# Kernel optimization log

Measured on AMD Instinct MI355X. Metric: run time of the kernel, lower is better.

Reference implementation:

```python
import jax, jax.numpy as jnp
import numpy as np

NU = 256      # numunits
NH = 32       # torch.split chunk size == head dim in this code
B = 128
S = 256


def _linear_tanh(x, W, b):
    # torch nn.Linear: y = x @ W.T + b, followed by tanh
    return jnp.tanh(x @ W.T + b)


def _split_heads(x):
    # torch.split(x, NH, dim=-1) then cat(dim=0): chunk c occupies rows [c*B, (c+1)*B)
    b, s, d = x.shape
    c = d // NH
    return x.reshape(b, s, c, NH).transpose(2, 0, 1, 3).reshape(c * b, s, NH)


def _merge_heads(x, b):
    # torch.split(x, batchsize, dim=0) then cat(dim=-1): inverse of _split_heads
    cb, s, hd = x.shape
    c = cb // b
    return x.reshape(c, b, s, hd).transpose(1, 2, 0, 3).reshape(b, s, c * hd)


def _attention(Q, K, V):
    d_k = jnp.asarray(K.shape[2], Q.dtype) ** 0.5
    scores = jnp.einsum('nqd,nkd->nqk', Q, K) / d_k
    # NB: original uses F.softmax(scores) with no dim on a 3D tensor ->
    # torch legacy default is dim=0. We reproduce that exactly.
    p_attn = jax.nn.softmax(scores, axis=0)
    return jnp.einsum('nqk,nkd->nqd', p_attn, V)


def setup_inputs() -> dict:
    key = jax.random.key(0)
    ks = jax.random.split(key, 24)
    def w(k):
        return jax.random.normal(k, (NU, NU), dtype=jnp.float32) * 0.02
    def bvec(k):
        return jax.random.normal(k, (NU,), dtype=jnp.float32) * 0.02
    inp = {
        'queries1': jax.random.normal(ks[0], (B, S, NU), dtype=jnp.float32),
        'queries2': jax.random.normal(ks[1], (B, S, NU), dtype=jnp.float32),
        'queries3': jax.random.normal(ks[2], (B, S, NU), dtype=jnp.float32),
        'adj': jax.random.randint(ks[3], (B,), 0, B, dtype=jnp.int64),
        'WQ': w(ks[4]),  'bQ': bvec(ks[5]),
        'WV': w(ks[6]),  'bV': bvec(ks[7]),
        'WQ3': w(ks[8]), 'bQ3': bvec(ks[9]),
        'WK3': w(ks[10]), 'bK3': bvec(ks[11]),
        'WV3': w(ks[12]), 'bV3': bvec(ks[13]),
        'WQ4': w(ks[14]), 'bQ4': bvec(ks[15]),
        'WV4': w(ks[16]), 'bV4': bvec(ks[17]),
        'W5': jax.random.normal(ks[18], (NU, 4 * NU), dtype=jnp.float32) * 0.02,
        'b5': bvec(ks[19]),
    }
    return inp


def reference(queries1, queries2, queries3, adj,
              WQ, bQ, WV, bV, WQ3, bQ3, WK3, bK3, WV3, bV3,
              WQ4, bQ4, WV4, bV4, W5, b5):
    b = queries1.shape[0]
    # per-row batch gather: queries4[i] = queries3[adj[i]]
    queries4 = queries3[adj]

    Q1 = _split_heads(_linear_tanh(queries1, WQ, bQ))
    Q2 = _split_heads(_linear_tanh(queries2, WQ, bQ))
    Q3 = _split_heads(_linear_tanh(queries3, WQ3, bQ3))
    Q4 = _split_heads(_linear_tanh(queries4, WQ4, bQ4))
    K3 = _split_heads(_linear_tanh(queries3, WK3, bK3))
    V1 = _split_heads(_linear_tanh(queries1, WV, bV))
    V2 = _split_heads(_linear_tanh(queries2, WV, bV))
    V3 = _split_heads(_linear_tanh(queries3, WV3, bV3))
    V4 = _split_heads(_linear_tanh(queries4, WV4, bV4))

    o1 = _merge_heads(_attention(Q1, K3, V1), b)
    o2 = _merge_heads(_attention(Q2, K3, V2), b)
    o3 = _merge_heads(_attention(Q3, K3, V3), b)
    o4 = _merge_heads(_attention(Q4, K3, V4), b)

    o5 = jnp.tanh(jnp.concatenate([o1, o2, o3, o4], axis=-1) @ W5.T + b5)
    return (o1, o2, o5, o3)
```

## Files before the change

kernel.cpp:

```cpp
#include <hip/hip_runtime.h>


typedef __attribute__((ext_vector_type(4))) float f32x4;
typedef __attribute__((ext_vector_type(8))) short bf16x8;

#define LOG2E 1.4426950408889634f
#define SM_SCALE (1.4426950408889634f / 5.656854249492381f)

#define CVT_PK(d, lo, hi) \
    asm("v_cvt_pk_bf16_f32 %0, %1, %2" : "=v"(d) : "v"(lo), "v"(hi))
#define SWAP32(x, y) \
    asm("v_permlane32_swap_b32 %0, %1" : "+v"(x), "+v"(y))
#define SWAP16(x, y) \
    asm("v_permlane16_swap_b32 %0, %1" : "+v"(x), "+v"(y))
#define GLOAD16(g, p) __builtin_amdgcn_global_load_lds( \
    (const __attribute__((address_space(1))) void*)(g), \
    (__attribute__((address_space(3))) void*)(p), 16, 0, 0)

__device__ __forceinline__ unsigned short f2bf(float x) {
    union { float f; unsigned u; } v; v.f = x;
    unsigned r = v.u + 0x7FFFu + ((v.u >> 16) & 1u);
    return (unsigned short)(r >> 16);
}

__device__ __forceinline__ float bf2f(unsigned short x) {
    union { unsigned u; float f; } v; v.u = ((unsigned)x) << 16;
    return v.f;
}

__device__ __forceinline__ float fast_tanh(float x) {
    float e = __builtin_amdgcn_exp2f(x * (2.0f * LOG2E));
    return 1.0f - 2.0f * __builtin_amdgcn_rcpf(e + 1.0f);
}

__device__ __forceinline__ f32x4 mfma_bf16(bf16x8 a, bf16x8 b, f32x4 c) {
    return __builtin_amdgcn_mfma_f32_16x16x32_bf16(a, b, c, 0, 0, 0);
}

__global__ __launch_bounds__(256) void k_convert_w(
    const float* w0, const float* w1, const float* w2, const float* w3,
    const float* w4, const float* w5, const float* w6, const float* w7,
    unsigned short* out)
{
    int i = blockIdx.x * 256 + threadIdx.x;
    if (i >= 720896) return;
    float v;
    if (i < 458752) {
        int r = i >> 16, j = i & 65535;
        const float* s =
            (r == 0) ? w0 : (r == 1) ? w1 : (r == 2) ? w2 :
            (r == 3) ? w3 : (r == 4) ? w4 : (r == 5) ? w5 : w6;
        v = s[j];
    } else {
        v = w7[i - 458752];
    }
    out[i] = (short)f2bf(v);
}

__global__ __launch_bounds__(256) void k_convert_x(
    const float* __restrict__ q1, const float* __restrict__ q2,
    const float* __restrict__ q3, unsigned short* __restrict__ Xb)
{
    const int gi = (blockIdx.x * 256 + threadIdx.x) * 8;
    const float* s = (gi < 8388608) ? q1 : (gi < 16777216) ? q2 : q3;
    const int off = gi & 8388607;
    float4 f0 = *(const float4*)(s + off);
    float4 f1 = *(const float4*)(s + off + 4);
    unsigned a0, a1, a2, a3;
    CVT_PK(a0, f0.x, f0.y);
    CVT_PK(a1, f0.z, f0.w);
    CVT_PK(a2, f1.x, f1.y);
    CVT_PK(a3, f1.z, f1.w);
    uint4 pk; pk.x = a0; pk.y = a1; pk.z = a2; pk.w = a3;
    *(uint4*)(Xb + gi) = pk;
}

__global__ __launch_bounds__(512, 4) void k_linear(
    const unsigned short* __restrict__ Xb, const int* __restrict__ adj,
    const unsigned short* __restrict__ wb,
    const float* __restrict__ bQ, const float* __restrict__ bV,
    const float* __restrict__ bQ3, const float* __restrict__ bK3,
    const float* __restrict__ bV3, const float* __restrict__ bQ4,
    const float* __restrict__ bV4,
    unsigned short* __restrict__ lin)
{
    __shared__ __align__(16) short lds[24576];
    const int bid0 = blockIdx.x;
    const int swz = (bid0 & 7) * 320 + (bid0 >> 3);
    const int var = swz >> 9;
    const int rem = swz & 511;
    const int m0 = (rem >> 1) * 128, n0 = (rem & 1) * 128;

    const unsigned short* X = Xb + (size_t)((var == 0) ? 0 : (var == 1) ? 1 : 2) * 8388608;
    const bool gather = (var == 4);
    const int nout = (var == 3) ? 1 : 2;

    int widx0, widx1 = 0, zidx0, zidx1 = 0;
    const float* bp0;
    const float* bp1 = bQ;
    if (var == 0)      { widx0=0; widx1=1; zidx0=0; zidx1=5; bp0=bQ;  bp1=bV;  }
    else if (var == 1) { widx0=0; widx1=1; zidx0=1; zidx1=6; bp0=bQ;  bp1=bV;  }
    else if (var == 2) { widx0=2; widx1=3; zidx0=2; zidx1=4; bp0=bQ3; bp1=bK3; }
    else if (var == 3) { widx0=4;          zidx0=7;          bp0=bV3;          }
    else               { widx0=5; widx1=6; zidx0=3; zidx1=8; bp0=bQ4; bp1=bV4; }

    const int tid = threadIdx.x;
    const int w = tid >> 6, l = tid & 63;
    const int wm = w >> 2, wn = w & 3;
    const int lr = l & 15, lk = (l >> 4) * 8, lq = (l >> 4) * 4;

    const int rowT = (w << 4) + (l >> 2);
    const int colT = (l & 3) << 3;
    const int gm = m0 + rowT;
    const int sm = gather ? (adj[gm >> 8] * 256 + (gm & 255)) : gm;
    const unsigned short* aG  = X + (size_t)sm * 256 + colT;
    const unsigned short* b0G = wb + (size_t)widx0 * 65536 + (size_t)(n0 + rowT) * 256 + colT;
    const unsigned short* b1G = wb + (size_t)widx1 * 65536 + (size_t)(n0 + rowT) * 256 + colT;
    char* ldsB = (char*)lds;
    const int wslice = w << 10;

    f32x4 acc[2][4][2] = {};

    GLOAD16(aG, ldsB + wslice);
    GLOAD16(b0G, ldsB + 8192 + wslice);
    if (nout == 2) GLOAD16(b1G, ldsB + 16384 + wslice);
    __syncthreads();

    for (int st = 0; st < 8; ++st) {
        const int p = st & 1;
        if (st < 7) {
            const int ko = (st + 1) * 32;
            char* nb = ldsB + (p ^ 1) * 24576;
            GLOAD16(aG + ko, nb + wslice);
            GLOAD16(b0G + ko, nb + 8192 + wslice);
            if (nout == 2) GLOAD16(b1G + ko, nb + 16384 + wslice);
        }
        const short* base = lds + p * 12288;
        bf16x8 af[4], bf0v[2], bf1v[2];
        #pragma unroll
        for (int i = 0; i < 4; ++i)
            af[i] = *(const bf16x8*)&base[(wm * 64 + i * 16 + lr) * 32 + lk];
        #pragma unroll
        for (int j = 0; j < 2; ++j)
            bf0v[j] = *(const bf16x8*)&base[4096 + (wn * 32 + j * 16 + lr) * 32 + lk];
        if (nout == 2)
            #pragma unroll
            for (int j = 0; j < 2; ++j)
                bf1v[j] = *(const bf16x8*)&base[8192 + (wn * 32 + j * 16 + lr) * 32 + lk];
        #pragma unroll
        for (int i = 0; i < 4; ++i)
            #pragma unroll
            for (int j = 0; j < 2; ++j)
                acc[0][i][j] = mfma_bf16(af[i], bf0v[j], acc[0][i][j]);
        if (nout == 2)
            #pragma unroll
            for (int i = 0; i < 4; ++i)
                #pragma unroll
                for (int j = 0; j < 2; ++j)
                    acc[1][i][j] = mfma_bf16(af[i], bf1v[j], acc[1][i][j]);
        __syncthreads();
    }

    #pragma unroll
    for (int t = 0; t < 2; ++t)
        if (t < nout) {
            const float* bp = t ? bp1 : bp0;
            const int zi = t ? zidx1 : zidx0;
            const float qs = (zi <= 3) ? SM_SCALE : 1.0f;
            float bv[2];
            #pragma unroll
            for (int j = 0; j < 2; ++j)
                bv[j] = bp[n0 + wn * 32 + j * 16 + lr];
            #pragma unroll
            for (int i = 0; i < 4; ++i)
                #pragma unroll
                for (int j = 0; j < 2; ++j)
                    #pragma unroll
                    for (int r = 0; r < 4; ++r)
                        lds[(wm * 64 + i * 16 + lq + r) * 136 + wn * 32 + j * 16 + lr] =
                            (short)f2bf(fast_tanh(acc[t][i][j][r] + bv[j]) * qs);
            __syncthreads();
            unsigned short* Y = lin + (size_t)zi * 8388608;
            #pragma unroll
            for (int it2 = 0; it2 < 4; ++it2) {
                const int c = tid + it2 * 512;
                const int row = c >> 4, col8 = (c & 15) * 8;
                *(bf16x8*)(Y + (size_t)(m0 + row) * 256 + n0 + col8) =
                    *(const bf16x8*)&lds[row * 136 + col8];
            }
            __syncthreads();
        }
}

__global__ __launch_bounds__(256) void k_denom(
    const unsigned short* __restrict__ Qa, const unsigned short* __restrict__ Qb2,
    const unsigned short* __restrict__ Qc, const unsigned short* __restrict__ Qd,
    const unsigned short* __restrict__ Kb, unsigned short* __restrict__ partial2)
{
    __shared__ __align__(16) short Qs[2][128 * 40];
    __shared__ __align__(16) short Ks[2][128 * 40];
    const int tid = threadIdx.x, w = tid >> 6, l = tid & 63;
    const int q0 = (blockIdx.x >> 1) * 128, k0 = (blockIdx.x & 1) * 128;
    const int g = blockIdx.y, a = blockIdx.z;
    const unsigned short* Qb = (a == 0) ? Qa : (a == 1) ? Qb2 : (a == 2) ? Qc : Qd;
    const int lr = l & 15, lk = (l >> 4) * 8;

    f32x4 eacc[2][8] = {};
    for (int it = 0; it < 32; it += 2) {
        __syncthreads();
        #pragma unroll
        for (int u = 0; u < 2; ++u) {
            const int n = g * 32 + it + u;
            const int c = n >> 7, b = n & 127;
            const size_t base = (size_t)b * 65536 + (size_t)c * 32;
            for (int ci = tid; ci < 512; ci += 256) {
                int r = ci >> 2, ch = ci & 3;
                *(bf16x8*)&Qs[u][r * 40 + ch * 8] =
                    *(const bf16x8*)(Qb + base + (size_t)(q0 + r) * 256 + ch * 8);
                *(bf16x8*)&Ks[u][r * 40 + ch * 8] =
                    *(const bf16x8*)(Kb + base + (size_t)(k0 + r) * 256 + ch * 8);
            }
        }
        __syncthreads();
        #pragma unroll
        for (int u = 0; u < 2; ++u) {
            bf16x8 aq[2], bk[8];
            #pragma unroll
            for (int i = 0; i < 2; ++i)
                aq[i] = *(const bf16x8*)&Qs[u][(w * 32 + i * 16 + lr) * 40 + lk];
            #pragma unroll
            for (int j = 0; j < 8; ++j)
                bk[j] = *(const bf16x8*)&Ks[u][(j * 16 + lr) * 40 + lk];
            #pragma unroll
            for (int i = 0; i < 2; ++i)
                #pragma unroll
                for (int j = 0; j < 8; ++j) {
                    f32x4 s = mfma_bf16(aq[i], bk[j], (f32x4){0.f, 0.f, 0.f, 0.f});
                    #pragma unroll
                    for (int r = 0; r < 4; ++r)
                        eacc[i][j][r] += __builtin_amdgcn_exp2f(s[r]);
                }
        }
    }
    const size_t pbase = (((size_t)a * 32 + g) << 16) + (size_t)blockIdx.x * 16384;
    #pragma unroll
    for (int cch = 0; cch < 8; ++cch) {
        const int ii = cch >> 2, jp = (cch & 3) * 2;
        union { unsigned short s[8]; bf16x8 v; } U;
        #pragma unroll
        for (int m = 0; m < 8; ++m)
            U.s[m] = f2bf(eacc[ii][jp + (m >> 2)][m & 3]);
        *(bf16x8*)&partial2[pbase + cch * 2048 + tid * 8] = U.v;
    }
}

__global__ __launch_bounds__(256) void k_reduce(
    const unsigned short* __restrict__ partial2, float* __restrict__ dinvP)
{
    const int a = blockIdx.y;
    const int gi = blockIdx.x * 256 + threadIdx.x;
    const unsigned short* p = partial2 + (size_t)a * 2097152 + gi;
    float s = 0.f;
    #pragma unroll
    for (int g = 0; g < 32; ++g) s += bf2f(p[(size_t)g * 65536]);
    const int tile = gi >> 14, rem2 = gi & 16383;
    const int cch = rem2 >> 11, tid2 = (rem2 >> 3) & 255, m = rem2 & 7;
    const int ii = cch >> 2, j = (cch & 3) * 2 + (m >> 2), r = m & 3;
    const int w2 = tid2 >> 6, l2 = tid2 & 63;
    const int q = (tile >> 1) * 128 + w2 * 32 + ii * 16 + ((l2 >> 4) * 4) + r;
    const int k = (tile & 1) * 128 + j * 16 + (l2 & 15);
    const int w_ = q >> 6, iq = (q >> 4) & 3, q16 = q & 15;
    const int kp = k >> 5, jj = (k >> 4) & 1, h = (k >> 2) & 3, rr = k & 3;
    const int off = (((((((w_ * 8 + kp) * 4 + iq) * 2 + jj) * 4 + h) * 16) + q16) * 4) + rr;
    dinvP[((size_t)a << 16) + off] = 1.0f / s;
}

__global__ __launch_bounds__(256) void k_attn(
    const unsigned short* __restrict__ Q1, const unsigned short* __restrict__ Q2,
    const unsigned short* __restrict__ Q3, const unsigned short* __restrict__ Q4,
    const unsigned short* __restrict__ Kb,
    const unsigned short* __restrict__ V1, const unsigned short* __restrict__ V2,
    const unsigned short* __restrict__ V3, const unsigned short* __restrict__ V4,
    const float* __restrict__ dinvP,
    float* __restrict__ outBase, unsigned short* __restrict__ ob4)
{
    __shared__ __align__(16) short Vt[32 * 264];
    __shared__ __align__(16) short Ks[256 * 40];
    const int tid = threadIdx.x, w = tid >> 6, l = tid & 63;
    const int bid = blockIdx.x;
    const int swz = (bid & 7) * 512 + (bid >> 3);
    const int a = swz & 3, n = swz >> 2;
    const int c = n >> 7, b = n & 127;
    const int q16 = l & 15, h = l >> 4;
    const size_t base = (size_t)b * 65536 + (size_t)c * 32;

    const unsigned short* Qb = (a == 0) ? Q1 : (a == 1) ? Q2 : (a == 2) ? Q3 : Q4;
    const unsigned short* Vb = (a == 0) ? V1 : (a == 1) ? V2 : (a == 2) ? V3 : V4;
    const f32x4* dw = (const f32x4*)(dinvP + ((size_t)a << 16)) + l + (size_t)w * 4096;
    float* outp = outBase + (size_t)((a == 2) ? 3 : a) * 8388608;

    {
        const unsigned short* vp = Vb + base + (size_t)tid * 256;
        const unsigned short* kp_ = Kb + base + (size_t)tid * 256;
        bf16x8 v0 = *(const bf16x8*)(vp);
        bf16x8 v1 = *(const bf16x8*)(vp + 8);
        bf16x8 v2 = *(const bf16x8*)(vp + 16);
        bf16x8 v3 = *(const bf16x8*)(vp + 24);
        bf16x8 k0 = *(const bf16x8*)(kp_);
        bf16x8 k1 = *(const bf16x8*)(kp_ + 8);
        bf16x8 k2 = *(const bf16x8*)(kp_ + 16);
        bf16x8 k3 = *(const bf16x8*)(kp_ + 24);
        *(bf16x8*)&Ks[tid * 40 + 0]  = k0;
        *(bf16x8*)&Ks[tid * 40 + 8]  = k1;
        *(bf16x8*)&Ks[tid * 40 + 16] = k2;
        *(bf16x8*)&Ks[tid * 40 + 24] = k3;
        #pragma unroll
        for (int e = 0; e < 8; ++e) {
            Vt[(0  + e) * 264 + tid] = v0[e];
            Vt[(8  + e) * 264 + tid] = v1[e];
            Vt[(16 + e) * 264 + tid] = v2[e];
            Vt[(24 + e) * 264 + tid] = v3[e];
        }
    }
    __syncthreads();

    const int q0 = w * 64;
    bf16x8 bq[4];
    #pragma unroll
    for (int i = 0; i < 4; ++i)
        bq[i] = *(const bf16x8*)(Qb + base + (size_t)(q0 + i * 16 + q16) * 256 + h * 8);

    f32x4 dc0 = dw[0];
    f32x4 dc1 = dw[64];

    f32x4 oacc[4][2] = {};
    for (int kp = 0; kp < 8; ++kp) {
        const int kk0 = kp * 32;
        bf16x8 akA = *(const bf16x8*)&Ks[(kk0 + q16) * 40 + h * 8];
        bf16x8 akB = *(const bf16x8*)&Ks[(kk0 + 16 + q16) * 40 + h * 8];
        bf16x8 vb0 = *(const bf16x8*)&Vt[(0  + q16) * 264 + kk0 + h * 8];
        bf16x8 vb1 = *(const bf16x8*)&Vt[(16 + q16) * 264 + kk0 + h * 8];
        #pragma unroll
        for (int i = 0; i < 4; ++i) {
            const int t = kp * 4 + i;
            f32x4 dn0 = dc0, dn1 = dc1;
            if (t < 31) {
                dn0 = dw[(size_t)(t + 1) * 128];
                dn1 = dw[(size_t)(t + 1) * 128 + 64];
            }
            __builtin_amdgcn_s_setprio(1);
            f32x4 s0 = mfma_bf16(akA, bq[i], (f32x4){0.f, 0.f, 0.f, 0.f});
            f32x4 s1 = mfma_bf16(akB, bq[i], (f32x4){0.f, 0.f, 0.f, 0.f});
            __builtin_amdgcn_s_setprio(0);
            float p0 = __builtin_amdgcn_exp2f(s0[0]) * dc0[0];
            float p1 = __builtin_amdgcn_exp2f(s0[1]) * dc0[1];
            float p2 = __builtin_amdgcn_exp2f(s0[2]) * dc0[2];
            float p3 = __builtin_amdgcn_exp2f(s0[3]) * dc0[3];
            float p4 = __builtin_amdgcn_exp2f(s1[0]) * dc1[0];
            float p5 = __builtin_amdgcn_exp2f(s1[1]) * dc1[1];
            float p6 = __builtin_amdgcn_exp2f(s1[2]) * dc1[2];
            float p7 = __builtin_amdgcn_exp2f(s1[3]) * dc1[3];
            unsigned r0, r1, r2, r3;
            CVT_PK(r0, p0, p1);
            CVT_PK(r1, p2, p3);
            CVT_PK(r2, p4, p5);
            CVT_PK(r3, p6, p7);
            SWAP32(r0, r2); SWAP16(r0, r2);
            SWAP32(r1, r3); SWAP16(r1, r3);
            union { unsigned u[4]; bf16x8 v; } F;
            F.u[0] = r0; F.u[1] = r1; F.u[2] = r2; F.u[3] = r3;
            __builtin_amdgcn_s_setprio(1);
            oacc[i][0] = mfma_bf16(F.v, vb0, oacc[i][0]);
            oacc[i][1] = mfma_bf16(F.v, vb1, oacc[i][1]);
            __builtin_amdgcn_s_setprio(0);
            dc0 = dn0; dc1 = dn1;
        }
    }
    if (a == 3) {
        #pragma unroll
        for (int i = 0; i < 4; ++i)
            #pragma unroll
            for (int d = 0; d < 2; ++d)
                #pragma unroll
                for (int r = 0; r < 4; ++r) {
                    int q = q0 + i * 16 + h * 4 + r;
                    int dc = d * 16 + q16;
                    ob4[(size_t)b * 65536 + (size_t)q * 256 + c * 32 + dc] =
                        f2bf(oacc[i][d][r]);
                }
    } else {
        #pragma unroll
        for (int i = 0; i < 4; ++i)
            #pragma unroll
            for (int d = 0; d < 2; ++d)
                #pragma unroll
                for (int r = 0; r < 4; ++r) {
                    int q = q0 + i * 16 + h * 4 + r;
                    int dc = d * 16 + q16;
                    outp[(size_t)b * 65536 + (size_t)q * 256 + c * 32 + dc] =
                        oacc[i][d][r];
                }
    }
}

__global__ __launch_bounds__(512, 2) void k_final(
    const float* __restrict__ p0, const float* __restrict__ p1,
    const float* __restrict__ p2, const unsigned short* __restrict__ p3,
    const unsigned short* __restrict__ W5b, const float* __restrict__ b5,
    float* __restrict__ out)
{
    __shared__ __align__(16) short As[128 * 72];
    __shared__ __align__(16) short Bs[256 * 72];
    const int tid = threadIdx.x, w = tid >> 6, l = tid & 63;
    const int wm = w >> 2, wn = w & 3;
    const int m0 = blockIdx.x * 128;
    const int lr = l & 15, lk = (l >> 4) * 8, lq = (l >> 4) * 4;

    f32x4 acc[4][4] = {};
    for (int step = 0; step < 16; ++step) {
        const int k0 = step * 64;
        const int kc = k0 & 255;
        __syncthreads();
        if (step < 12) {
            const float* P = (step < 4) ? p0 : (step < 8) ? p1 : p2;
            #pragma unroll
            for (int it = 0; it < 2; ++it) {
                const int cc = tid + it * 512;
                const int row = cc >> 3, ch = cc & 7;
                const float* src = P + (size_t)(m0 + row) * 256 + kc + ch * 8;
                float4 f0 = *(const float4*)src;
                float4 f1 = *(const float4*)(src + 4);
                unsigned a0, a1, a2, a3;
                CVT_PK(a0, f0.x, f0.y);
                CVT_PK(a1, f0.z, f0.w);
                CVT_PK(a2, f1.x, f1.y);
                CVT_PK(a3, f1.z, f1.w);
                uint4 pk; pk.x = a0; pk.y = a1; pk.z = a2; pk.w = a3;
                *(uint4*)&As[row * 72 + ch * 8] = pk;
            }
        } else {
            #pragma unroll
            for (int it = 0; it < 2; ++it) {
                const int cc = tid + it * 512;
                const int row = cc >> 3, ch = cc & 7;
                *(bf16x8*)&As[row * 72 + ch * 8] =
                    *(const bf16x8*)(p3 + (size_t)(m0 + row) * 256 + kc + ch * 8);
            }
        }
        #pragma unroll
        for (int it = 0; it < 4; ++it) {
            const int cc = tid + it * 512;
            const int row = cc >> 3, ch = cc & 7;
            *(bf16x8*)&Bs[row * 72 + ch * 8] =
                *(const bf16x8*)(W5b + (size_t)row * 1024 + k0 + ch * 8);
        }
        __syncthreads();
        #pragma unroll
        for (int kk = 0; kk < 2; ++kk) {
            bf16x8 af[4], bfr[4];
            #pragma unroll
            for (int i = 0; i < 4; ++i)
                af[i] = *(const bf16x8*)&As[(wm * 64 + i * 16 + lr) * 72 + kk * 32 + lk];
            #pragma unroll
            for (int j = 0; j < 4; ++j)
                bfr[j] = *(const bf16x8*)&Bs[(wn * 64 + j * 16 + lr) * 72 + kk * 32 + lk];
            #pragma unroll
            for (int i = 0; i < 4; ++i)
                #pragma unroll
                for (int j = 0; j < 4; ++j)
                    acc[i][j] = mfma_bf16(af[i], bfr[j], acc[i][j]);
        }
    }
    #pragma unroll
    for (int j = 0; j < 4; ++j) {
        int col = wn * 64 + j * 16 + lr;
        float bv = b5[col];
        #pragma unroll
        for (int i = 0; i < 4; ++i) {
            int rowb = m0 + wm * 64 + i * 16 + lq;
            #pragma unroll
            for (int r = 0; r < 4; ++r)
                out[(size_t)(rowb + r) * 256 + col] =
                    fast_tanh(acc[i][j][r] + bv);
        }
    }
}

extern "C" void kernel_launch(void* const* d_in, const int* in_sizes, int n_in,
                              void* d_out, int out_size, void* d_ws, size_t ws_size,
                              hipStream_t stream)
{
    const float* q1  = (const float*)d_in[0];
    const float* q2  = (const float*)d_in[1];
    const float* q3  = (const float*)d_in[2];
    const int*   adj = (const int*)d_in[3];
    const float* WQ  = (const float*)d_in[4];  const float* bQ  = (const float*)d_in[5];
    const float* WV  = (const float*)d_in[6];  const float* bV  = (const float*)d_in[7];
    const float* WQ3 = (const float*)d_in[8];  const float* bQ3 = (const float*)d_in[9];
    const float* WK3 = (const float*)d_in[10]; const float* bK3 = (const float*)d_in[11];
    const float* WV3 = (const float*)d_in[12]; const float* bV3 = (const float*)d_in[13];
    const float* WQ4 = (const float*)d_in[14]; const float* bQ4 = (const float*)d_in[15];
    const float* WV4 = (const float*)d_in[16]; const float* bV4 = (const float*)d_in[17];
    const float* W5  = (const float*)d_in[18]; const float* b5  = (const float*)d_in[19];

    char* ws = (char*)d_ws;
    unsigned short* wb  = (unsigned short*)ws;
    unsigned short* W5b = wb + 458752;
    unsigned short* lin = (unsigned short*)(ws + 1441792);
    unsigned short* Q1 = lin + 0ull * 8388608;
    unsigned short* Q2 = lin + 1ull * 8388608;
    unsigned short* Q3 = lin + 2ull * 8388608;
    unsigned short* Q4 = lin + 3ull * 8388608;
    unsigned short* K3 = lin + 4ull * 8388608;
    unsigned short* V1 = lin + 5ull * 8388608;
    unsigned short* V2 = lin + 6ull * 8388608;
    unsigned short* V3 = lin + 7ull * 8388608;
    unsigned short* V4 = lin + 8ull * 8388608;
    unsigned short* partial2 = (unsigned short*)(ws + 152436736);
    float* dinvP   = (float*)(ws + 185991168);
    unsigned short* ob4 = (unsigned short*)(ws + 152436736);

    float* outf = (float*)d_out;
    float* o5p = outf + 2ull * 8388608;
    unsigned short* Xb = (unsigned short*)d_out;

    dim3 blk(256);

    hipLaunchKernelGGL(k_convert_w, dim3(2816), blk, 0, stream,
                       WQ, WV, WQ3, WK3, WV3, WQ4, WV4, W5, wb);
    hipLaunchKernelGGL(k_convert_x, dim3(12288), blk, 0, stream,
                       q1, q2, q3, Xb);

    hipLaunchKernelGGL(k_linear, dim3(2560), dim3(512), 0, stream,
                       Xb, adj, wb,
                       bQ, bV, bQ3, bK3, bV3, bQ4, bV4, lin);

    hipLaunchKernelGGL(k_denom, dim3(4, 32, 4), blk, 0, stream,
                       Q1, Q2, Q3, Q4, K3, partial2);
    hipLaunchKernelGGL(k_reduce, dim3(256, 4), blk, 0, stream, partial2, dinvP);

    hipLaunchKernelGGL(k_attn, dim3(4096), blk, 0, stream,
                       Q1, Q2, Q3, Q4, K3, V1, V2, V3, V4, dinvP,
                       outf, ob4);

    hipLaunchKernelGGL(k_final, dim3(256), dim3(512), 0, stream,
                       outf, outf + 8388608ull, outf + 3ull * 8388608, ob4,
                       W5b, b5, o5p);
}
```

Before: 288.1 us.

## Double-buffer k_denom Q/K tiles with async global-to-LDS loads

Replaces the synchronous register-staged Q/K tile loads in the softmax-denominator kernel with global_load_lds direct-to-LDS copies into a double buffer. The next head slice is prefetched while MFMA and exp2 work runs on the current one, and each iteration now needs a single barrier instead of two per pair of slices. The padded stride-40 LDS layout is dropped for an unpadded stride-32 layout, which may add LDS bank conflicts on the fragment reads. The loop also stops processing two slices per iteration.

```diff
diff --git a/kernel.cpp b/kernel.cpp
--- a/kernel.cpp
+++ b/kernel.cpp
@@ -197,51 +197,58 @@
     const unsigned short* __restrict__ Qc, const unsigned short* __restrict__ Qd,
     const unsigned short* __restrict__ Kb, unsigned short* __restrict__ partial2)
 {
-    __shared__ __align__(16) short Qs[2][128 * 40];
-    __shared__ __align__(16) short Ks[2][128 * 40];
+    __shared__ __align__(16) short lds[2][8192];
     const int tid = threadIdx.x, w = tid >> 6, l = tid & 63;
     const int q0 = (blockIdx.x >> 1) * 128, k0 = (blockIdx.x & 1) * 128;
     const int g = blockIdx.y, a = blockIdx.z;
     const unsigned short* Qb = (a == 0) ? Qa : (a == 1) ? Qb2 : (a == 2) ? Qc : Qd;
     const int lr = l & 15, lk = (l >> 4) * 8;
 
+    const int rowA = (w << 4) + (l >> 2);
+    const int colA = (l & 3) << 3;
+    char* ldsB = (char*)lds;
+    const int wsl = w << 10;
+
+    #define NBASE(nn) ((size_t)((nn) & 127) * 65536 + (size_t)((nn) >> 7) * 32)
+    #define STAGE(bf, nn) do {                                                   \
+        const size_t bs_ = NBASE(nn);                                            \
+        char* d_ = ldsB + (bf) * 16384;                                          \
+        GLOAD16(Qb + bs_ + (size_t)(q0 + rowA) * 256 + colA,      d_ + wsl);     \
+        GLOAD16(Qb + bs_ + (size_t)(q0 + rowA + 64) * 256 + colA, d_ + 4096 + wsl); \
+        GLOAD16(Kb + bs_ + (size_t)(k0 + rowA) * 256 + colA,      d_ + 8192 + wsl); \
+        GLOAD16(Kb + bs_ + (size_t)(k0 + rowA + 64) * 256 + colA, d_ + 12288 + wsl); \
+    } while (0)
+
+    STAGE(0, g * 32);
+    __syncthreads();
+
     f32x4 eacc[2][8] = {};
-    for (int it = 0; it < 32; it += 2) {
+    for (int it = 0; it < 32; ++it) {
+        const int buf = it & 1;
+        if (it < 31) STAGE(buf ^ 1, g * 32 + it + 1);
+        const short* qs = lds[buf];
+        const short* ks = lds[buf] + 4096;
+        bf16x8 aq[2], bk[8];
+        #pragma unroll
+        for (int i = 0; i < 2; ++i)
+            aq[i] = *(const bf16x8*)&qs[(w * 32 + i * 16 + lr) * 32 + lk];
+        #pragma unroll
+        for (int j = 0; j < 8; ++j)
+            bk[j] = *(const bf16x8*)&ks[(j * 16 + lr) * 32 + lk];
+        #pragma unroll
+        for (int i = 0; i < 2; ++i)
+            #pragma unroll
+            for (int j = 0; j < 8; ++j) {
+                f32x4 s = mfma_bf16(aq[i], bk[j], (f32x4){0.f, 0.f, 0.f, 0.f});
+                #pragma unroll
+                for (int r = 0; r < 4; ++r)
+                    eacc[i][j][r] += __builtin_amdgcn_exp2f(s[r]);
+            }
         __syncthreads();
-        #pragma unroll
-        for (int u = 0; u < 2; ++u) {
-            const int n = g * 32 + it + u;
-            const int c = n >> 7, b = n & 127;
-            const size_t base = (size_t)b * 65536 + (size_t)c * 32;
-            for (int ci = tid; ci < 512; ci += 256) {
-                int r = ci >> 2, ch = ci & 3;
-                *(bf16x8*)&Qs[u][r * 40 + ch * 8] =
-                    *(const bf16x8*)(Qb + base + (size_t)(q0 + r) * 256 + ch * 8);
-                *(bf16x8*)&Ks[u][r * 40 + ch * 8] =
-                    *(const bf16x8*)(Kb + base + (size_t)(k0 + r) * 256 + ch * 8);
-            }
-        }
-        __syncthreads();
-        #pragma unroll
-        for (int u = 0; u < 2; ++u) {
-            bf16x8 aq[2], bk[8];
-            #pragma unroll
-            for (int i = 0; i < 2; ++i)
-                aq[i] = *(const bf16x8*)&Qs[u][(w * 32 + i * 16 + lr) * 40 + lk];
-            #pragma unroll
-            for (int j = 0; j < 8; ++j)
-                bk[j] = *(const bf16x8*)&Ks[u][(j * 16 + lr) * 40 + lk];
-            #pragma unroll
-            for (int i = 0; i < 2; ++i)
-                #pragma unroll
-                for (int j = 0; j < 8; ++j) {
-                    f32x4 s = mfma_bf16(aq[i], bk[j], (f32x4){0.f, 0.f, 0.f, 0.f});
-                    #pragma unroll
-                    for (int r = 0; r < 4; ++r)
-                        eacc[i][j][r] += __builtin_amdgcn_exp2f(s[r]);
-                }
-        }
-    }
+    }
+    #undef STAGE
+    #undef NBASE
+
     const size_t pbase = (((size_t)a * 32 + g) << 16) + (size_t)blockIdx.x * 16384;
     #pragma unroll
     for (int cch = 0; cch < 8; ++cch) {
```

Result: no change. 284.7 us (median of 2 runs) (-1.2%).
